# Performance work log

Measured on AMD Instinct MI355X. Metric: run time of the kernel, lower is better.

## Reference

```python
import jax, jax.numpy as jnp
import numpy as np

N_NODES = 100000


def _sage_conv(x, src, dst, W_l, b_l, W_r, num_nodes):
    # PyG SAGEConv (aggr='mean'): out = lin_l(mean_j x_j) + lin_r(x)
    msg = x[src]                                                   # [E, d] gather
    s = jax.ops.segment_sum(msg, dst, num_segments=num_nodes)      # [N, d]
    cnt = jax.ops.segment_sum(jnp.ones((src.shape[0], 1), x.dtype), dst,
                              num_segments=num_nodes)              # [N, 1]
    agg = s / jnp.maximum(cnt, 1)                                  # mean, 0 if no neighbors
    return agg @ W_l.T + b_l + x @ W_r.T


def setup_inputs() -> dict:
    key = jax.random.key(0)
    ks = jax.random.split(key, 8)
    d = 64
    E = 1600000
    scale = 1.0 / np.sqrt(d)
    x = jax.random.normal(ks[0], (N_NODES, d), dtype=jnp.float32)
    edge_index = jax.random.randint(ks[1], (2, E), 0, N_NODES, dtype=jnp.int64)
    W1_l = jax.random.normal(ks[2], (d, d), dtype=jnp.float32) * scale
    b1_l = jnp.zeros((d,), dtype=jnp.float32)
    W1_r = jax.random.normal(ks[3], (d, d), dtype=jnp.float32) * scale
    W2_l = jax.random.normal(ks[4], (d, d), dtype=jnp.float32) * scale
    b2_l = jnp.zeros((d,), dtype=jnp.float32)
    W2_r = jax.random.normal(ks[5], (d, d), dtype=jnp.float32) * scale
    return {"x": x, "edge_index": edge_index, "W1_l": W1_l, "b1_l": b1_l,
            "W1_r": W1_r, "W2_l": W2_l, "b2_l": b2_l, "W2_r": W2_r}


def reference(x, edge_index, W1_l, b1_l, W1_r, W2_l, b2_l, W2_r):
    src, dst = edge_index[0], edge_index[1]
    h = jax.nn.relu(_sage_conv(x, src, dst, W1_l, b1_l, W1_r, N_NODES))
    h = jax.nn.relu(_sage_conv(h, src, dst, W2_l, b2_l, W2_r, N_NODES))
    return h
```

## Files before the change

### kernel.cpp

```cpp
#include <hip/hip_runtime.h>
#include <hip/hip_fp16.h>


#define NFEAT 64
#define NPB 128
#define NBUCK 782
#define MAXPB 2560
#define TILE 4096

typedef _Float16 h8 __attribute__((ext_vector_type(8)));
typedef _Float16 h4 __attribute__((ext_vector_type(4)));
typedef float f4 __attribute__((ext_vector_type(4)));
typedef float f2 __attribute__((ext_vector_type(2)));

__device__ inline h8 cvt8f(const float* p) {
  float4 lo = *(const float4*)p;
  float4 hi = *(const float4*)(p + 4);
  h8 f;
  f[0]=(_Float16)lo.x; f[1]=(_Float16)lo.y; f[2]=(_Float16)lo.z; f[3]=(_Float16)lo.w;
  f[4]=(_Float16)hi.x; f[5]=(_Float16)hi.y; f[6]=(_Float16)hi.z; f[7]=(_Float16)hi.w;
  return f;
}

__device__ inline void acc16(float* a, uint4 r) {
  f2 t;
  t = __builtin_amdgcn_cvt_pk_f32_fp8((int)r.x, false); a[0]+=t[0];  a[1]+=t[1];
  t = __builtin_amdgcn_cvt_pk_f32_fp8((int)r.x, true);  a[2]+=t[0];  a[3]+=t[1];
  t = __builtin_amdgcn_cvt_pk_f32_fp8((int)r.y, false); a[4]+=t[0];  a[5]+=t[1];
  t = __builtin_amdgcn_cvt_pk_f32_fp8((int)r.y, true);  a[6]+=t[0];  a[7]+=t[1];
  t = __builtin_amdgcn_cvt_pk_f32_fp8((int)r.z, false); a[8]+=t[0];  a[9]+=t[1];
  t = __builtin_amdgcn_cvt_pk_f32_fp8((int)r.z, true);  a[10]+=t[0]; a[11]+=t[1];
  t = __builtin_amdgcn_cvt_pk_f32_fp8((int)r.w, false); a[12]+=t[0]; a[13]+=t[1];
  t = __builtin_amdgcn_cvt_pk_f32_fp8((int)r.w, true);  a[14]+=t[0]; a[15]+=t[1];
}

__global__ __launch_bounds__(512) void build_gemm1_k(
    const int* __restrict__ src, const int* __restrict__ dst,
    int* __restrict__ gcur, int* __restrict__ pairs, int E, int sb,
    const float* __restrict__ X, const float* __restrict__ Wl,
    const float* __restrict__ Wr, const float* __restrict__ bias,
    unsigned char* __restrict__ Zf8, __half* __restrict__ Ph, int n) {
  int tid = threadIdx.x;
  if ((int)blockIdx.x < sb) {
    __shared__ int lcnt[NBUCK];
    __shared__ int loff[NBUCK];
    __shared__ int lcur[NBUCK];
    __shared__ int lbase[NBUCK];
    __shared__ int s_packed[TILE];
    __shared__ unsigned short s_b[TILE];

    int tileStart = blockIdx.x * TILE;
    int tileCnt = E - tileStart; if (tileCnt > TILE) tileCnt = TILE;

    for (int t = tid; t < NBUCK; t += 512) lcnt[t] = 0;
    __syncthreads();

    int ep[8], eb[8];
    int base = tileStart + tid * 8;
    int ne = 0;
    if (base + 7 < E) {
      int4 a0 = *(const int4*)(src + base);
      int4 a1 = *(const int4*)(src + base + 4);
      int4 b0 = *(const int4*)(dst + base);
      int4 b1 = *(const int4*)(dst + base + 4);
      int es[8] = {a0.x,a0.y,a0.z,a0.w,a1.x,a1.y,a1.z,a1.w};
      int ed[8] = {b0.x,b0.y,b0.z,b0.w,b1.x,b1.y,b1.z,b1.w};
#pragma unroll
      for (int j = 0; j < 8; ++j) {
        eb[j] = ed[j] >> 7;
        ep[j] = es[j] | ((ed[j] & 127) << 17);
      }
      ne = 8;
    } else {
      for (int j = 0; j < 8 && base + j < E; ++j) {
        int s = src[base + j], d = dst[base + j];
        eb[j] = d >> 7;
        ep[j] = s | ((d & 127) << 17);
        ++ne;
      }
    }
    for (int j = 0; j < ne; ++j) atomicAdd(&lcnt[eb[j]], 1);
    __syncthreads();

    if (tid < 64) {
      int carry = 0;
      for (int cb = 0; cb < NBUCK; cb += 64) {
        int i = cb + tid;
        int v = (i < NBUCK) ? lcnt[i] : 0;
        int x = v;
#pragma unroll
        for (int d = 1; d < 64; d <<= 1) {
          int y = __shfl_up(x, d);
          if (tid >= d) x += y;
        }
        if (i < NBUCK) { int e = x - v + carry; loff[i] = e; lcur[i] = e; }
        carry += __shfl(x, 63);
      }
    }
    __syncthreads();

    for (int t = tid; t < NBUCK; t += 512) {
      int v = lcnt[t];
      if (v) lbase[t] = atomicAdd(&gcur[t], v);
    }
    __syncthreads();

    for (int j = 0; j < ne; ++j) {
      int b = eb[j];
      int slot = atomicAdd(&lcur[b], 1);
      s_packed[slot] = ep[j];
      s_b[slot] = (unsigned short)b;
    }
    __syncthreads();

    for (int k = tid; k < tileCnt; k += 512) {
      int b = s_b[k];
      int g = lbase[b] + (k - loff[b]);
      if (g < MAXPB) pairs[(size_t)b * MAXPB + g] = s_packed[k];
    }
  } else {
    int wave = tid >> 6, lane = tid & 63;
    int m = lane & 15, quad = lane >> 4;
    int row0 = (((int)blockIdx.x - sb) * 8 + wave) * 16;
    if (row0 >= n) return;

    h8 wf[2][4][2];
#pragma unroll
    for (int mat = 0; mat < 2; ++mat) {
      const float* W = mat ? Wr : Wl;
#pragma unroll
      for (int t = 0; t < 4; ++t)
#pragma unroll
        for (int s = 0; s < 2; ++s)
          wf[mat][t][s] = cvt8f(W + (t * 16 + m) * 64 + s * 32 + quad * 8);
    }

    int rowm = row0 + m; if (rowm > n - 1) rowm = n - 1;
    const float* xp = X + (size_t)rowm * 64 + quad * 8;
    h8 af0 = cvt8f(xp);
    h8 af1 = cvt8f(xp + 32);

    f4 accz[4], accp[4];
#pragma unroll
    for (int t = 0; t < 4; ++t) {
      f4 z; z[0]=0.f; z[1]=0.f; z[2]=0.f; z[3]=0.f;
      float4 bl = *(const float4*)(bias + t * 16 + quad * 4);
      f4 p; p[0]=bl.x; p[1]=bl.y; p[2]=bl.z; p[3]=bl.w;
      z = __builtin_amdgcn_mfma_f32_16x16x32_f16(wf[0][t][0], af0, z, 0, 0, 0);
      z = __builtin_amdgcn_mfma_f32_16x16x32_f16(wf[0][t][1], af1, z, 0, 0, 0);
      p = __builtin_amdgcn_mfma_f32_16x16x32_f16(wf[1][t][0], af0, p, 0, 0, 0);
      p = __builtin_amdgcn_mfma_f32_16x16x32_f16(wf[1][t][1], af1, p, 0, 0, 0);
      accz[t] = z;
      accp[t] = p;
    }

    if (row0 + m < n) {
      size_t node = (size_t)(row0 + m);
#pragma unroll
      for (int t = 0; t < 4; ++t) {
        h4 pv;
#pragma unroll
        for (int r = 0; r < 4; ++r) pv[r] = (_Float16)accp[t][r];
        *(h4*)(Ph + node * NFEAT + t * 16 + quad * 4) = pv;
        int v = 0;
        v = __builtin_amdgcn_cvt_pk_fp8_f32(accz[t][0], accz[t][1], v, false);
        v = __builtin_amdgcn_cvt_pk_fp8_f32(accz[t][2], accz[t][3], v, true);
        *(int*)(Zf8 + node * NFEAT + t * 16 + quad * 4) = v;
      }
    }
  }
}

__global__ __launch_bounds__(512) void raggemm_k(
    const int* __restrict__ gcur, const int* __restrict__ pairs,
    int* __restrict__ csr, int* __restrict__ off,
    int* __restrict__ cnt, float* __restrict__ inv,
    const unsigned char* __restrict__ Z, const __half* __restrict__ Pin,
    const float* __restrict__ Wl, const float* __restrict__ Wr,
    const float* __restrict__ bias,
    unsigned char* __restrict__ Zout, __half* __restrict__ Pout, int n) {
  __shared__ int lcnt[NPB];
  __shared__ int lofs[NPB];
  __shared__ int lcur[NPB];
  __shared__ int stage[MAXPB];
  __shared__ _Float16 Hs[NPB][72];

  int tid = threadIdx.x;
  int b = blockIdx.x;
  int nbase = b << 7;
  int nn = n - nbase; if (nn > NPB) nn = NPB;
  if (nn <= 0) return;

  int m = gcur[b]; if (m > MAXPB) m = MAXPB;
  const int* seg = pairs + (size_t)b * MAXPB;

  if (tid < NPB) lcnt[tid] = 0;
  __syncthreads();

  for (int e = tid; e < m; e += 512)
    atomicAdd(&lcnt[(seg[e] >> 17) & 127], 1);
  __syncthreads();

  if (tid < 64) {
    int carry = 0;
#pragma unroll
    for (int cb = 0; cb < NPB; cb += 64) {
      int i = cb + tid;
      int v = lcnt[i];
      int x = v;
#pragma unroll
      for (int d = 1; d < 64; d <<= 1) {
        int y = __shfl_up(x, d);
        if (tid >= d) x += y;
      }
      int e = x - v + carry;
      lofs[i] = e; lcur[i] = e;
      carry += __shfl(x, 63);
    }
  }
  __syncthreads();

  for (int e = tid; e < m; e += 512) {
    int p = seg[e];
    int slot = atomicAdd(&lcur[(p >> 17) & 127], 1);
    stage[slot] = p & 0x1FFFF;
  }
  __syncthreads();

  for (int k = tid; k < m; k += 512) csr[(size_t)b * MAXPB + k] = stage[k];
  for (int t = tid; t < nn; t += 512) {
    int c = lcnt[t];
    cnt[nbase + t] = c;
    off[nbase + t] = b * MAXPB + lofs[t];
    inv[nbase + t] = 1.0f / (float)(c > 1 ? c : 1);
  }

  int nl = tid >> 2;
  int q  = tid & 3;
  int node = nbase + nl;

  h8 h0, h1;
  if (node < n) {
    float a[16];
#pragma unroll
    for (int i = 0; i < 16; ++i) a[i] = 0.f;
    int deg = lcnt[nl];
    int start = lofs[nl];
    int j = 0;
    for (; j + 4 <= deg; j += 4) {
      int n0 = stage[start + j + 0];
      int n1 = stage[start + j + 1];
      int n2 = stage[start + j + 2];
      int n3 = stage[start + j + 3];
      uint4 r0 = *(const uint4*)(Z + (size_t)n0 * NFEAT + q * 16);
      uint4 r1 = *(const uint4*)(Z + (size_t)n1 * NFEAT + q * 16);
      uint4 r2 = *(const uint4*)(Z + (size_t)n2 * NFEAT + q * 16);
      uint4 r3 = *(const uint4*)(Z + (size_t)n3 * NFEAT + q * 16);
      acc16(a, r0); acc16(a, r1); acc16(a, r2); acc16(a, r3);
    }
    for (; j < deg; ++j) {
      int nb = stage[start + j];
      uint4 r = *(const uint4*)(Z + (size_t)nb * NFEAT + q * 16);
      acc16(a, r);
    }
    float iv = 1.0f / (float)(deg > 1 ? deg : 1);
    h8 p0 = *(const h8*)(Pin + (size_t)node * NFEAT + q * 16);
    h8 p1 = *(const h8*)(Pin + (size_t)node * NFEAT + q * 16 + 8);
#pragma unroll
    for (int i = 0; i < 8; ++i)
      h0[i] = (_Float16)fmaxf(fmaf(a[i], iv, (float)p0[i]), 0.f);
#pragma unroll
    for (int i = 0; i < 8; ++i)
      h1[i] = (_Float16)fmaxf(fmaf(a[8 + i], iv, (float)p1[i]), 0.f);
  } else {
#pragma unroll
    for (int i = 0; i < 8; ++i) { h0[i] = (_Float16)0.f; h1[i] = (_Float16)0.f; }
  }
  *(h8*)&Hs[nl][q * 16] = h0;
  *(h8*)&Hs[nl][q * 16 + 8] = h1;

  int wave = tid >> 6, lane = tid & 63;
  int mm = lane & 15, quad = lane >> 4;
  int row0 = wave * 16;

  h8 wf[2][4][2];
#pragma unroll
  for (int mat = 0; mat < 2; ++mat) {
    const float* W = mat ? Wr : Wl;
#pragma unroll
    for (int t = 0; t < 4; ++t)
#pragma unroll
      for (int s = 0; s < 2; ++s)
        wf[mat][t][s] = cvt8f(W + (t * 16 + mm) * 64 + s * 32 + quad * 8);
  }

  h8 af0 = *(const h8*)&Hs[row0 + mm][quad * 8];
  h8 af1 = *(const h8*)&Hs[row0 + mm][32 + quad * 8];

  f4 accz[4], accp[4];
#pragma unroll
  for (int t = 0; t < 4; ++t) {
    f4 z; z[0]=0.f; z[1]=0.f; z[2]=0.f; z[3]=0.f;
    float4 bl = *(const float4*)(bias + t * 16 + quad * 4);
    f4 p; p[0]=bl.x; p[1]=bl.y; p[2]=bl.z; p[3]=bl.w;
    z = __builtin_amdgcn_mfma_f32_16x16x32_f16(wf[0][t][0], af0, z, 0, 0, 0);
    z = __builtin_amdgcn_mfma_f32_16x16x32_f16(wf[0][t][1], af1, z, 0, 0, 0);
    p = __builtin_amdgcn_mfma_f32_16x16x32_f16(wf[1][t][0], af0, p, 0, 0, 0);
    p = __builtin_amdgcn_mfma_f32_16x16x32_f16(wf[1][t][1], af1, p, 0, 0, 0);
    accz[t] = z;
    accp[t] = p;
  }

  int gnode = nbase + row0 + mm;
  if (gnode < n) {
    size_t nodeix = (size_t)gnode;
#pragma unroll
    for (int t = 0; t < 4; ++t) {
      h4 pv;
#pragma unroll
      for (int r = 0; r < 4; ++r) pv[r] = (_Float16)accp[t][r];
      *(h4*)(Pout + nodeix * NFEAT + t * 16 + quad * 4) = pv;
      int v = 0;
      v = __builtin_amdgcn_cvt_pk_fp8_f32(accz[t][0], accz[t][1], v, false);
      v = __builtin_amdgcn_cvt_pk_fp8_f32(accz[t][2], accz[t][3], v, true);
      *(int*)(Zout + nodeix * NFEAT + t * 16 + quad * 4) = v;
    }
  }
}

__global__ __launch_bounds__(256) void agg2_k(const int* __restrict__ off,
                                              const int* __restrict__ cnt,
                                              const float* __restrict__ inv,
                                              const int* __restrict__ csr,
                                              const unsigned char* __restrict__ Z,
                                              const __half* __restrict__ Pin,
                                              float* __restrict__ out, int n) {
  int t = blockIdx.x * 256 + threadIdx.x;
  int node = t >> 2;
  if (node >= n) return;
  int q = t & 3;

  float a[16];
#pragma unroll
  for (int i = 0; i < 16; ++i) a[i] = 0.f;

  int start = off[node];
  int deg = cnt[node];
  int j = 0;
  for (; j + 4 <= deg; j += 4) {
    int n0 = csr[start + j + 0];
    int n1 = csr[start + j + 1];
    int n2 = csr[start + j + 2];
    int n3 = csr[start + j + 3];
    uint4 r0 = *(const uint4*)(Z + (size_t)n0 * NFEAT + q * 16);
    uint4 r1 = *(const uint4*)(Z + (size_t)n1 * NFEAT + q * 16);
    uint4 r2 = *(const uint4*)(Z + (size_t)n2 * NFEAT + q * 16);
    uint4 r3 = *(const uint4*)(Z + (size_t)n3 * NFEAT + q * 16);
    acc16(a, r0); acc16(a, r1); acc16(a, r2); acc16(a, r3);
  }
  for (; j < deg; ++j) {
    int nb = csr[start + j];
    uint4 r = *(const uint4*)(Z + (size_t)nb * NFEAT + q * 16);
    acc16(a, r);
  }

  float iv = inv[node];
  h8 p0 = *(const h8*)(Pin + (size_t)node * NFEAT + q * 16);
  h8 p1 = *(const h8*)(Pin + (size_t)node * NFEAT + q * 16 + 8);

  float4 r0, r1, r2, r3;
  r0.x = fmaxf(fmaf(a[0],  iv, (float)p0[0]), 0.f);
  r0.y = fmaxf(fmaf(a[1],  iv, (float)p0[1]), 0.f);
  r0.z = fmaxf(fmaf(a[2],  iv, (float)p0[2]), 0.f);
  r0.w = fmaxf(fmaf(a[3],  iv, (float)p0[3]), 0.f);
  r1.x = fmaxf(fmaf(a[4],  iv, (float)p0[4]), 0.f);
  r1.y = fmaxf(fmaf(a[5],  iv, (float)p0[5]), 0.f);
  r1.z = fmaxf(fmaf(a[6],  iv, (float)p0[6]), 0.f);
  r1.w = fmaxf(fmaf(a[7],  iv, (float)p0[7]), 0.f);
  r2.x = fmaxf(fmaf(a[8],  iv, (float)p1[0]), 0.f);
  r2.y = fmaxf(fmaf(a[9],  iv, (float)p1[1]), 0.f);
  r2.z = fmaxf(fmaf(a[10], iv, (float)p1[2]), 0.f);
  r2.w = fmaxf(fmaf(a[11], iv, (float)p1[3]), 0.f);
  r3.x = fmaxf(fmaf(a[12], iv, (float)p1[4]), 0.f);
  r3.y = fmaxf(fmaf(a[13], iv, (float)p1[5]), 0.f);
  r3.z = fmaxf(fmaf(a[14], iv, (float)p1[6]), 0.f);
  r3.w = fmaxf(fmaf(a[15], iv, (float)p1[7]), 0.f);

  float* op = out + (size_t)node * NFEAT + q * 16;
  *(float4*)(op + 0)  = r0;
  *(float4*)(op + 4)  = r1;
  *(float4*)(op + 8)  = r2;
  *(float4*)(op + 12) = r3;
}

extern "C" void kernel_launch(void* const* d_in, const int* in_sizes, int n_in,
                              void* d_out, int out_size, void* d_ws, size_t ws_size,
                              hipStream_t stream) {
  const float* x   = (const float*)d_in[0];
  const int*   ei  = (const int*)d_in[1];
  const float* W1l = (const float*)d_in[2];
  const float* b1  = (const float*)d_in[3];
  const float* W1r = (const float*)d_in[4];
  const float* W2l = (const float*)d_in[5];
  const float* b2  = (const float*)d_in[6];
  const float* W2r = (const float*)d_in[7];
  float* out = (float*)d_out;

  int N = in_sizes[0] / NFEAT;
  int E = in_sizes[1] / 2;
  const int* srcp = ei;
  const int* dstp = ei + E;

  char* w = (char*)d_ws;
  int*           pairs = (int*)w;           w += (size_t)NBUCK * MAXPB * 4;
  int*           csr   = (int*)w;           w += (size_t)NBUCK * MAXPB * 4;
  unsigned char* Z1    = (unsigned char*)w; w += (size_t)N * NFEAT;
  __half*        P1    = (__half*)w;        w += (size_t)N * NFEAT * 2;
  unsigned char* Z2    = (unsigned char*)w; w += (size_t)N * NFEAT;
  __half*        P2    = (__half*)w;        w += (size_t)N * NFEAT * 2;
  int*           off   = (int*)w;           w += (size_t)N * 4;
  int*           cnt   = (int*)w;           w += (size_t)N * 4;
  float*         inv   = (float*)w;         w += (size_t)N * 4;
  int*           gcur  = (int*)w;           w += NBUCK * 4;
  if ((size_t)(w - (char*)d_ws) > ws_size) return;

  hipMemsetAsync(gcur, 0, NBUCK * 4, stream);

  int sb  = (E + TILE - 1) / TILE;
  int gb1 = (N + 127) / 128;

  build_gemm1_k<<<sb + gb1, 512, 0, stream>>>(srcp, dstp, gcur, pairs, E, sb,
                                              x, W1l, W1r, b1, Z1, P1, N);
  raggemm_k<<<NBUCK, 512, 0, stream>>>(gcur, pairs, csr, off, cnt, inv,
                                       Z1, P1, W2l, W2r, b2, Z2, P2, N);
  agg2_k<<<(N * 4 + 255) / 256, 256, 0, stream>>>(off, cnt, inv, csr, Z2, P2,
                                                  out, N);
}
```

Before: 227.0 us.

## Double edge tile size and parallelize bucket scan across all waves

Each bucketing block now handles 8192 edges, 16 per thread, so there are half as many blocks and fewer global atomics on the bucket cursors. The exclusive scan over 782 buckets is split across 8 waves, each scanning 98 buckets, followed by a small cross-wave offset pass, instead of a single wave doing the whole scan serially. This costs more LDS per block and more registers per thread, which may lower occupancy and lengthen the per-block local sort.

New measurement: 225.5 us. About the same (-0.7%).

```diff
diff --git a/kernel.cpp b/kernel.cpp
--- a/kernel.cpp
+++ b/kernel.cpp
@@ -6,7 +6,7 @@
 #define NPB 128
 #define NBUCK 782
 #define MAXPB 2560
-#define TILE 4096
+#define TILE 8192
 
 typedef _Float16 h8 __attribute__((ext_vector_type(8)));
 typedef _Float16 h4 __attribute__((ext_vector_type(4)));
@@ -46,6 +46,8 @@
     __shared__ int loff[NBUCK];
     __shared__ int lcur[NBUCK];
     __shared__ int lbase[NBUCK];
+    __shared__ int wtot[8];
+    __shared__ int wbase[8];
     __shared__ int s_packed[TILE];
     __shared__ unsigned short s_b[TILE];
 
@@ -55,24 +57,25 @@
     for (int t = tid; t < NBUCK; t += 512) lcnt[t] = 0;
     __syncthreads();
 
-    int ep[8], eb[8];
-    int base = tileStart + tid * 8;
+    int ep[16], eb[16];
+    int base = tileStart + tid * 16;
     int ne = 0;
-    if (base + 7 < E) {
-      int4 a0 = *(const int4*)(src + base);
-      int4 a1 = *(const int4*)(src + base + 4);
-      int4 b0 = *(const int4*)(dst + base);
-      int4 b1 = *(const int4*)(dst + base + 4);
-      int es[8] = {a0.x,a0.y,a0.z,a0.w,a1.x,a1.y,a1.z,a1.w};
-      int ed[8] = {b0.x,b0.y,b0.z,b0.w,b1.x,b1.y,b1.z,b1.w};
-#pragma unroll
-      for (int j = 0; j < 8; ++j) {
-        eb[j] = ed[j] >> 7;
-        ep[j] = es[j] | ((ed[j] & 127) << 17);
+    if (base + 15 < E) {
+#pragma unroll
+      for (int c = 0; c < 4; ++c) {
+        int4 a = *(const int4*)(src + base + c * 4);
+        int4 b = *(const int4*)(dst + base + c * 4);
+        int es[4] = {a.x, a.y, a.z, a.w};
+        int ed[4] = {b.x, b.y, b.z, b.w};
+#pragma unroll
+        for (int j = 0; j < 4; ++j) {
+          eb[c * 4 + j] = ed[j] >> 7;
+          ep[c * 4 + j] = es[j] | ((ed[j] & 127) << 17);
+        }
       }
-      ne = 8;
+      ne = 16;
     } else {
-      for (int j = 0; j < 8 && base + j < E; ++j) {
+      for (int j = 0; j < 16 && base + j < E; ++j) {
         int s = src[base + j], d = dst[base + j];
         eb[j] = d >> 7;
         ep[j] = s | ((d & 127) << 17);
@@ -82,20 +85,35 @@
     for (int j = 0; j < ne; ++j) atomicAdd(&lcnt[eb[j]], 1);
     __syncthreads();
 
-    if (tid < 64) {
+    {
+      int wv = tid >> 6, ln = tid & 63;
+      int wstart = wv * 98;
+      int wend = wstart + 98; if (wend > NBUCK) wend = NBUCK;
       int carry = 0;
-      for (int cb = 0; cb < NBUCK; cb += 64) {
-        int i = cb + tid;
-        int v = (i < NBUCK) ? lcnt[i] : 0;
+      for (int cb = wstart; cb < wend; cb += 64) {
+        int i = cb + ln;
+        int v = (i < wend) ? lcnt[i] : 0;
         int x = v;
 #pragma unroll
         for (int d = 1; d < 64; d <<= 1) {
           int y = __shfl_up(x, d);
-          if (tid >= d) x += y;
+          if (ln >= d) x += y;
         }
-        if (i < NBUCK) { int e = x - v + carry; loff[i] = e; lcur[i] = e; }
+        if (i < wend) loff[i] = x - v + carry;
         carry += __shfl(x, 63);
       }
+      if (ln == 0) wtot[wv] = carry;
+    }
+    __syncthreads();
+    if (tid == 0) {
+      int s = 0;
+#pragma unroll
+      for (int i = 0; i < 8; ++i) { wbase[i] = s; s += wtot[i]; }
+    }
+    __syncthreads();
+    for (int t = tid; t < NBUCK; t += 512) {
+      int e = loff[t] + wbase[t / 98];
+      loff[t] = e; lcur[t] = e;
     }
     __syncthreads();
 
```
